# Performance work log

Hardware: AMD Instinct MI355X
Metric: run time of the kernel (lower is better)

## Reference

```python
import jax, jax.numpy as jnp
import numpy as np

EPS = 1e-5
QB = 128.0  # 2**(bit-1), bit=8

def _int8_wrap(q):
    # Emulate torch's .to(torch.int8) two's-complement wrap (e.g. 128 -> -128).
    return jnp.mod(q + 128.0, 256.0) - 128.0

def setup_inputs() -> dict:
    key = jax.random.key(0)
    k1, k2, k3 = jax.random.split(key, 3)
    x = jax.random.normal(k1, (4, 2048, 2048), dtype=jnp.float32)
    weights = jax.random.normal(k2, (8192, 2048), dtype=jnp.float32)
    bias = jax.random.normal(k3, (8192,), dtype=jnp.float32)
    return {"x": x, "weights": weights, "bias": bias}

def reference(x, weights, bias):
    in_features = x.shape[-1]
    out_features = weights.shape[0]
    # LayerNorm over last dim, no affine (F.layer_norm defaults, eps=1e-5)
    mu = jnp.mean(x, axis=-1, keepdims=True)
    var = jnp.mean(jnp.square(x - mu), axis=-1, keepdims=True)
    input_norm = (x - mu) * jax.lax.rsqrt(var + EPS)
    # absmax int8 activation quant (nl_next=False path)
    max_val = jnp.max(jnp.abs(input_norm))
    q = _int8_wrap(jnp.round(input_norm * (QB / max_val)))
    dequant = max_val / QB
    # weight sign-binarization around the mean
    weight_quant = jnp.sign(weights - jnp.mean(weights))
    # quantized matmul + dequant scales + bias
    out = jnp.einsum('bsd,od->bso', q, weight_quant)  # [B,S,out]
    beta = jnp.sum(jnp.abs(weights)) / (in_features * out_features)
    out = out * (dequant * beta) + bias
    return out
```

## Files before the change

kernel.cpp:

```cpp
#include <hip/hip_runtime.h>


using i32x4 = __attribute__((ext_vector_type(4))) int;

typedef const __attribute__((address_space(1))) void cg_void;
typedef __attribute__((address_space(3))) void lds_void;

#define K_DIM 2048
#define N_DIM 8192
#define M_DIM 8192
#define NELEM_W 16777216


__global__ __launch_bounds__(256) void pass1(const float* __restrict__ x,
                                             const float4* __restrict__ w4,
                                             float* __restrict__ mu_arr,
                                             float* __restrict__ rstd_arr,
                                             float* __restrict__ rowmax,
                                             double2* __restrict__ part) {
    __shared__ double sbd[8];
    __shared__ float sb1[4];
    __shared__ float sb2[8];
    const int bid = blockIdx.x, t = threadIdx.x;
    const int lane = t & 63, wv = t >> 6;
    if (bid < 1024) {
        double s = 0.0, a = 0.0;
        for (int i = bid * 256 + t; i < NELEM_W / 4; i += 1024 * 256) {
            float4 v = w4[i];
            s += (double)v.x + (double)v.y + (double)v.z + (double)v.w;
            a += fabs((double)v.x) + fabs((double)v.y) + fabs((double)v.z) + fabs((double)v.w);
        }
        for (int o = 32; o; o >>= 1) { s += __shfl_xor(s, o); a += __shfl_xor(a, o); }
        if (lane == 0) { sbd[wv] = s; sbd[4 + wv] = a; }
        __syncthreads();
        if (t == 0) {
            double2 r;
            r.x = sbd[0] + sbd[1] + sbd[2] + sbd[3];
            r.y = sbd[4] + sbd[5] + sbd[6] + sbd[7];
            part[bid] = r;
        }
    } else {
        const int row = bid - 1024;
        const float4* xr = (const float4*)x + (size_t)row * 512;
        float4 v0 = xr[t], v1 = xr[t + 256];
        float s = v0.x + v0.y + v0.z + v0.w + v1.x + v1.y + v1.z + v1.w;
        for (int o = 32; o; o >>= 1) s += __shfl_xor(s, o);
        if (lane == 0) sb1[wv] = s;
        __syncthreads();
        float mu = (sb1[0] + sb1[1] + sb1[2] + sb1[3]) * (1.0f / 2048.0f);
        float ssq = 0.f, md = 0.f, d;
        d = v0.x - mu; ssq += d * d; md = fmaxf(md, fabsf(d));
        d = v0.y - mu; ssq += d * d; md = fmaxf(md, fabsf(d));
        d = v0.z - mu; ssq += d * d; md = fmaxf(md, fabsf(d));
        d = v0.w - mu; ssq += d * d; md = fmaxf(md, fabsf(d));
        d = v1.x - mu; ssq += d * d; md = fmaxf(md, fabsf(d));
        d = v1.y - mu; ssq += d * d; md = fmaxf(md, fabsf(d));
        d = v1.z - mu; ssq += d * d; md = fmaxf(md, fabsf(d));
        d = v1.w - mu; ssq += d * d; md = fmaxf(md, fabsf(d));
        for (int o = 32; o; o >>= 1) {
            ssq += __shfl_xor(ssq, o);
            md = fmaxf(md, __shfl_xor(md, o));
        }
        if (lane == 0) { sb2[wv] = ssq; sb2[4 + wv] = md; }
        __syncthreads();
        if (t == 0) {
            float var = (sb2[0] + sb2[1] + sb2[2] + sb2[3]) * (1.0f / 2048.0f);
            float rstd = 1.0f / sqrtf(var + 1e-5f);
            mu_arr[row] = mu;
            rstd_arr[row] = rstd;
            rowmax[row] = fmaxf(fmaxf(sb2[4], sb2[5]), fmaxf(sb2[6], sb2[7])) * rstd;
        }
    }
}

__global__ __launch_bounds__(256) void wred2(const double2* __restrict__ part,
                                             const float* __restrict__ rowmax,
                                             unsigned* __restrict__ scal) {
    double s = 0.0, a = 0.0;
    float m = 0.f;
    const int t = threadIdx.x, lane = t & 63, wv = t >> 6;
    for (int i = t; i < 1024; i += 256) { double2 p = part[i]; s += p.x; a += p.y; }
    for (int i = t; i < 8192; i += 256) m = fmaxf(m, rowmax[i]);
    for (int o = 32; o; o >>= 1) {
        s += __shfl_xor(s, o); a += __shfl_xor(a, o);
        m = fmaxf(m, __shfl_xor(m, o));
    }
    __shared__ double sbd[8];
    __shared__ float sbm[4];
    if (lane == 0) { sbd[wv] = s; sbd[4 + wv] = a; sbm[wv] = m; }
    __syncthreads();
    if (t == 0) {
        double st = sbd[0] + sbd[1] + sbd[2] + sbd[3];
        double at = sbd[4] + sbd[5] + sbd[6] + sbd[7];
        ((float*)scal)[0] = fmaxf(fmaxf(sbm[0], sbm[1]), fmaxf(sbm[2], sbm[3]));
        ((float*)scal)[1] = (float)(st / (double)NELEM_W);
        ((float*)scal)[2] = (float)(at / (double)NELEM_W);
    }
}

__device__ __forceinline__ int sgn8(float d) { return (d > 0.f) ? 1 : ((d < 0.f) ? -1 : 0); }

__global__ __launch_bounds__(256) void pass2(const float* __restrict__ x,
                                             const float4* __restrict__ w4,
                                             const float* __restrict__ mu_arr,
                                             const float* __restrict__ rstd_arr,
                                             const unsigned* __restrict__ scal,
                                             signed char* __restrict__ q,
                                             int4* __restrict__ wq4) {
    const int bid = blockIdx.x, t = threadIdx.x;
    if (bid < 1024) {
        float wm = ((const float*)scal)[1];
        for (int i = bid * 256 + t; i < NELEM_W / 16; i += 1024 * 256) {
            int words[4];
            #pragma unroll
            for (int jj = 0; jj < 4; ++jj) {
                float4 v = w4[i * 4 + jj];
                int b0 = sgn8(v.x - wm) & 255, b1 = sgn8(v.y - wm) & 255;
                int b2 = sgn8(v.z - wm) & 255, b3 = sgn8(v.w - wm) & 255;
                words[jj] = b0 | (b1 << 8) | (b2 << 16) | (b3 << 24);
            }
            wq4[i] = make_int4(words[0], words[1], words[2], words[3]);
        }
    } else {
        const int row = bid - 1024;
        float mu = mu_arr[row], rstd = rstd_arr[row];
        float s = 128.0f / ((const float*)scal)[0];
        const float4* xr = (const float4*)x + (size_t)row * 512;
        float4 v0 = xr[2 * t], v1 = xr[2 * t + 1];
        float xs[8] = {v0.x, v0.y, v0.z, v0.w, v1.x, v1.y, v1.z, v1.w};
        int b[8];
        #pragma unroll
        for (int j = 0; j < 8; ++j) {
            float norm = (xs[j] - mu) * rstd;
            int qi = (int)rintf(norm * s);
            b[j] = qi & 255;
        }
        int w0 = b[0] | (b[1] << 8) | (b[2] << 16) | (b[3] << 24);
        int w1 = b[4] | (b[5] << 8) | (b[6] << 16) | (b[7] << 24);
        ((int2*)(q + (size_t)row * 2048))[t] = make_int2(w0, w1);
    }
}

#define LD16(p) (*(const i32x4*)(p))

#define STAGE(aoff, boff, sbase)                                                            \
    do {                                                                                    \
        _Pragma("unroll") for (int i_ = 0; i_ < 4; ++i_)                                    \
            __builtin_amdgcn_global_load_lds((cg_void*)(gA + (size_t)i_ * 131072 + (aoff)), \
                (lds_void*)(lds + (sbase) + i_ * 8192 + w * 1024), 16, 0, 0);               \
        _Pragma("unroll") for (int i_ = 0; i_ < 4; ++i_)                                    \
            __builtin_amdgcn_global_load_lds((cg_void*)(gB + (size_t)i_ * 131072 + (boff)), \
                (lds_void*)(lds + (sbase) + 32768 + i_ * 8192 + w * 1024), 16, 0, 0);       \
    } while (0)

#define MFC(MB, AF, BF)                                                                     \
    __builtin_amdgcn_s_setprio(1);                                                          \
    _Pragma("unroll") for (int mm = 0; mm < 4; ++mm)                                        \
        _Pragma("unroll") for (int nn = 0; nn < 4; ++nn)                                    \
            acc[(MB) + mm][nn] = __builtin_amdgcn_mfma_i32_16x16x64_i8(                     \
                AF[mm], BF[nn], acc[(MB) + mm][nn], 0, 0, 0);                               \
    __builtin_amdgcn_s_setprio(0);

__global__ __launch_bounds__(512, 2) void gemm_i8(const signed char* __restrict__ A,
                                                  const signed char* __restrict__ B,
                                                  const float* __restrict__ bias,
                                                  const unsigned* __restrict__ scal,
                                                  float* __restrict__ C) {
    __shared__ alignas(16) char lds[131072];
    const int t = threadIdx.x, w = t >> 6, lane = t & 63;

    const int wg = blockIdx.x;
    const int xcd = wg & 7, j = wg >> 3;
    const int bm = (xcd * 4 + (j >> 3)) * 256;
    const int col0 = (j & 7) * 4;

    const int wr = w >> 2, wc = w & 3;
    const int r16 = lane & 15, ko = lane >> 4;

    const int srow = w * 8 + (lane >> 3);
    const int scol = ((lane & 7) ^ (lane >> 3)) << 4;
    const signed char* gA = A + (size_t)(bm + srow) * K_DIM + scol;
    const signed char* gB = B + (size_t)(col0 * 256 + srow) * K_DIM + scol;

    const char* aBase = lds + (wr * 128 + r16) * 128;
    const char* bBase = lds + 32768 + (wc * 64 + r16) * 128;
    const int xr = (r16 & 7) << 4;
    const int sw0 = (ko * 16) ^ xr;
    const int sw1 = (64 + ko * 16) ^ xr;

    const float scale = (((const float*)scal)[0] * (1.0f / 128.0f)) * ((const float*)scal)[2];

    i32x4 acc[8][4] = {};
    i32x4 a0[4], a1[4], b0[4], b1[4];

    STAGE(0, 0, 0);

    #pragma unroll 2
    for (int gt = 0; gt < 64; ++gt) {
        const int c = (gt & 1) << 16;
        if (gt < 63) {
            const int nt = gt + 1;
            const int kt1 = nt & 15, rep1 = nt >> 4;
            const size_t aoff = (size_t)(kt1 * 128);
            const size_t boff = (size_t)rep1 * 524288 + (size_t)(kt1 * 128);
            STAGE(aoff, boff, (nt & 1) << 16);
            asm volatile("s_waitcnt vmcnt(8)" ::: "memory");
        } else {
            asm volatile("s_waitcnt vmcnt(0)" ::: "memory");
        }
        __builtin_amdgcn_s_barrier();

        #pragma unroll
        for (int m = 0; m < 4; ++m) a0[m] = LD16(aBase + c + m * 2048 + sw0);
        #pragma unroll
        for (int n = 0; n < 4; ++n) b0[n] = LD16(bBase + c + n * 2048 + sw0);
        #pragma unroll
        for (int m = 0; m < 4; ++m) a1[m] = LD16(aBase + c + (4 + m) * 2048 + sw0);
        MFC(0, a0, b0);
        #pragma unroll
        for (int m = 0; m < 4; ++m) a0[m] = LD16(aBase + c + m * 2048 + sw1);
        #pragma unroll
        for (int n = 0; n < 4; ++n) b1[n] = LD16(bBase + c + n * 2048 + sw1);
        MFC(4, a1, b0);
        #pragma unroll
        for (int m = 0; m < 4; ++m) a1[m] = LD16(aBase + c + (4 + m) * 2048 + sw1);
        MFC(0, a0, b1);
        MFC(4, a1, b1);
        __builtin_amdgcn_s_barrier();

        if ((gt & 15) == 15) {
            const int rep = gt >> 4;
            const int colbase = (col0 + rep) * 256 + wc * 64;
            float bi[4];
            #pragma unroll
            for (int n = 0; n < 4; ++n) bi[n] = bias[colbase + n * 16 + r16];
            #pragma unroll
            for (int m = 0; m < 8; ++m) {
                #pragma unroll
                for (int n = 0; n < 4; ++n) {
                    #pragma unroll
                    for (int r = 0; r < 4; ++r) {
                        int row = bm + wr * 128 + m * 16 + ko * 4 + r;
                        int col = colbase + n * 16 + r16;
                        C[(size_t)row * N_DIM + col] = (float)acc[m][n][r] * scale + bi[n];
                    }
                }
            }
            #pragma unroll
            for (int m = 0; m < 8; ++m)
                #pragma unroll
                for (int n = 0; n < 4; ++n) acc[m][n] = (i32x4){0, 0, 0, 0};
        }
    }
}

extern "C" void kernel_launch(void* const* d_in, const int* in_sizes, int n_in,
                              void* d_out, int out_size, void* d_ws, size_t ws_size,
                              hipStream_t stream) {
    const float* x = (const float*)d_in[0];
    const float* wts = (const float*)d_in[1];
    const float* bias = (const float*)d_in[2];
    float* out = (float*)d_out;

    char* ws = (char*)d_ws;
    unsigned* scal = (unsigned*)ws;
    double2* part = (double2*)(ws + 1024);
    float* mu = (float*)(ws + 32768);
    float* rstd = (float*)(ws + 65536);
    float* rowmax = (float*)(ws + 98304);
    signed char* q = (signed char*)(ws + 131072);
    signed char* wq = (signed char*)(ws + 131072 + 16777216);

    hipLaunchKernelGGL(pass1, dim3(9216), dim3(256), 0, stream,
                       x, (const float4*)wts, mu, rstd, rowmax, part);
    hipLaunchKernelGGL(wred2, dim3(1), dim3(256), 0, stream, part, rowmax, scal);
    hipLaunchKernelGGL(pass2, dim3(9216), dim3(256), 0, stream,
                       x, (const float4*)wts, mu, rstd, scal, q, (int4*)wq);
    hipLaunchKernelGGL(gemm_i8, dim3(256), dim3(512), 0, stream,
                       q, wq, bias, scal, out);
}
```

Measured before the change: 253.4 us.

## Switch int8 GEMM to 32x32x32 MFMA with barrier-separated K phases

Replaces the 16x16x64 int8 MFMA tiling with 32x32x32 int8 MFMAs accumulating into 16-wide vectors. The per-wave tile stays 128x64 but uses fewer, larger instructions and fewer fragment loads. Each 128-wide K slice is split into four phases, each with an LDS fragment load, a full lgkmcnt wait and a workgroup barrier. The larger MFMA is meant to raise throughput per LDS byte, but the extra barriers and waits limit overlap of LDS reads with math. The epilogue row and column mapping is rewritten for the 32x32 output layout.

```diff
diff --git a/kernel.cpp b/kernel.cpp
--- a/kernel.cpp
+++ b/kernel.cpp
@@ -2,6 +2,7 @@
 
 
 using i32x4 = __attribute__((ext_vector_type(4))) int;
+using i32x16 = __attribute__((ext_vector_type(16))) int;
 
 typedef const __attribute__((address_space(1))) void cg_void;
 typedef __attribute__((address_space(3))) void lds_void;
@@ -153,13 +154,22 @@
                 (lds_void*)(lds + (sbase) + 32768 + i_ * 8192 + w * 1024), 16, 0, 0);       \
     } while (0)
 
-#define MFC(MB, AF, BF)                                                                     \
-    __builtin_amdgcn_s_setprio(1);                                                          \
-    _Pragma("unroll") for (int mm = 0; mm < 4; ++mm)                                        \
-        _Pragma("unroll") for (int nn = 0; nn < 4; ++nn)                                    \
-            acc[(MB) + mm][nn] = __builtin_amdgcn_mfma_i32_16x16x64_i8(                     \
-                AF[mm], BF[nn], acc[(MB) + mm][nn], 0, 0, 0);                               \
-    __builtin_amdgcn_s_setprio(0);
+#define PHASE32(KOFF, LEAD_BAR)                                                             \
+    do {                                                                                    \
+        _Pragma("unroll") for (int mb = 0; mb < 4; ++mb)                                    \
+            af[mb] = LD16(aB + mb * 4096 + (KOFF));                                         \
+        _Pragma("unroll") for (int nb = 0; nb < 2; ++nb)                                    \
+            bf[nb] = LD16(bB + nb * 4096 + (KOFF));                                         \
+        if (LEAD_BAR) __builtin_amdgcn_s_barrier();                                         \
+        asm volatile("s_waitcnt lgkmcnt(0)" ::: "memory");                                  \
+        __builtin_amdgcn_s_setprio(1);                                                      \
+        _Pragma("unroll") for (int mb = 0; mb < 4; ++mb)                                    \
+            _Pragma("unroll") for (int nb = 0; nb < 2; ++nb)                                 \
+                acc[mb][nb] = __builtin_amdgcn_mfma_i32_32x32x32_i8(                        \
+                    af[mb], bf[nb], acc[mb][nb], 0, 0, 0);                                  \
+        __builtin_amdgcn_s_setprio(0);                                                      \
+        __builtin_amdgcn_s_barrier();                                                       \
+    } while (0)
 
 __global__ __launch_bounds__(512, 2) void gemm_i8(const signed char* __restrict__ A,
                                                   const signed char* __restrict__ B,
@@ -175,23 +185,25 @@
     const int col0 = (j & 7) * 4;
 
     const int wr = w >> 2, wc = w & 3;
-    const int r16 = lane & 15, ko = lane >> 4;
+    const int r32 = lane & 31, hi = lane >> 5;
 
     const int srow = w * 8 + (lane >> 3);
     const int scol = ((lane & 7) ^ (lane >> 3)) << 4;
     const signed char* gA = A + (size_t)(bm + srow) * K_DIM + scol;
     const signed char* gB = B + (size_t)(col0 * 256 + srow) * K_DIM + scol;
 
-    const char* aBase = lds + (wr * 128 + r16) * 128;
-    const char* bBase = lds + 32768 + (wc * 64 + r16) * 128;
-    const int xr = (r16 & 7) << 4;
-    const int sw0 = (ko * 16) ^ xr;
-    const int sw1 = (64 + ko * 16) ^ xr;
+    const char* aBase = lds + (wr * 128 + r32) * 128;
+    const char* bBase = lds + 32768 + (wc * 64 + r32) * 128;
+    const int xr32 = (r32 & 7) << 4;
+    const int kf0 = (0 * 32 + hi * 16) ^ xr32;
+    const int kf1 = (1 * 32 + hi * 16) ^ xr32;
+    const int kf2 = (2 * 32 + hi * 16) ^ xr32;
+    const int kf3 = (3 * 32 + hi * 16) ^ xr32;
 
     const float scale = (((const float*)scal)[0] * (1.0f / 128.0f)) * ((const float*)scal)[2];
 
-    i32x4 acc[8][4] = {};
-    i32x4 a0[4], a1[4], b0[4], b1[4];
+    i32x16 acc[4][2] = {};
+    i32x4 af[4], bf[2];
 
     STAGE(0, 0, 0);
 
@@ -210,46 +222,35 @@
         }
         __builtin_amdgcn_s_barrier();
 
-        #pragma unroll
-        for (int m = 0; m < 4; ++m) a0[m] = LD16(aBase + c + m * 2048 + sw0);
-        #pragma unroll
-        for (int n = 0; n < 4; ++n) b0[n] = LD16(bBase + c + n * 2048 + sw0);
-        #pragma unroll
-        for (int m = 0; m < 4; ++m) a1[m] = LD16(aBase + c + (4 + m) * 2048 + sw0);
-        MFC(0, a0, b0);
-        #pragma unroll
-        for (int m = 0; m < 4; ++m) a0[m] = LD16(aBase + c + m * 2048 + sw1);
-        #pragma unroll
-        for (int n = 0; n < 4; ++n) b1[n] = LD16(bBase + c + n * 2048 + sw1);
-        MFC(4, a1, b0);
-        #pragma unroll
-        for (int m = 0; m < 4; ++m) a1[m] = LD16(aBase + c + (4 + m) * 2048 + sw1);
-        MFC(0, a0, b1);
-        MFC(4, a1, b1);
-        __builtin_amdgcn_s_barrier();
+        const char* aB = aBase + c;
+        const char* bB = bBase + c;
+        PHASE32(kf0, 0);
+        PHASE32(kf1, 1);
+        PHASE32(kf2, 1);
+        PHASE32(kf3, 1);
 
         if ((gt & 15) == 15) {
             const int rep = gt >> 4;
             const int colbase = (col0 + rep) * 256 + wc * 64;
-            float bi[4];
-            #pragma unroll
-            for (int n = 0; n < 4; ++n) bi[n] = bias[colbase + n * 16 + r16];
-            #pragma unroll
-            for (int m = 0; m < 8; ++m) {
+            float bi[2];
+            #pragma unroll
+            for (int nb = 0; nb < 2; ++nb) bi[nb] = bias[colbase + nb * 32 + r32];
+            #pragma unroll
+            for (int mb = 0; mb < 4; ++mb) {
                 #pragma unroll
-                for (int n = 0; n < 4; ++n) {
+                for (int nb = 0; nb < 2; ++nb) {
                     #pragma unroll
-                    for (int r = 0; r < 4; ++r) {
-                        int row = bm + wr * 128 + m * 16 + ko * 4 + r;
-                        int col = colbase + n * 16 + r16;
-                        C[(size_t)row * N_DIM + col] = (float)acc[m][n][r] * scale + bi[n];
+                    for (int r = 0; r < 16; ++r) {
+                        int row = bm + wr * 128 + mb * 32 + (r & 3) + 8 * (r >> 2) + 4 * hi;
+                        int col = colbase + nb * 32 + r32;
+                        C[(size_t)row * N_DIM + col] = (float)acc[mb][nb][r] * scale + bi[nb];
                     }
                 }
             }
             #pragma unroll
-            for (int m = 0; m < 8; ++m)
+            for (int mb = 0; mb < 4; ++mb)
                 #pragma unroll
-                for (int n = 0; n < 4; ++n) acc[m][n] = (i32x4){0, 0, 0, 0};
+                for (int nb = 0; nb < 2; ++nb) acc[mb][nb] = (i32x16){};
         }
     }
 }
```

After: 255.6 us. No clear change (+0.9%).

## Retile int8 GEMM to 256x128 blocks with 32x32x32 MFMA and higher occupancy

Applied to the files above, without the earlier changes.

Replaces the persistent 256x1024 block tiling (256 blocks looping over four 256-column sweeps, 128 KB LDS) with 2048 smaller blocks of 256x128 output and a K-step of 64, using 48 KB LDS and launch bounds allowing four blocks per CU. The inner product switches from 16x16x64 to 32x32x32 int8 MFMA with a new swizzle and 64-byte LDS rows, and the epilogue runs once after the K loop. The aim is more resident waves to hide memory latency and simpler scheduling. In exchange, operand reuse per LDS byte drops and the B matrix is reloaded by many more blocks, raising global and L2 traffic.

```diff
diff --git a/kernel.cpp b/kernel.cpp
--- a/kernel.cpp
+++ b/kernel.cpp
@@ -2,6 +2,7 @@
 
 
 using i32x4 = __attribute__((ext_vector_type(4))) int;
+using i32x16 = __attribute__((ext_vector_type(16))) int;
 
 typedef const __attribute__((address_space(1))) void cg_void;
 typedef __attribute__((address_space(3))) void lds_void;
@@ -142,114 +143,102 @@
 }
 
 #define LD16(p) (*(const i32x4*)(p))
-
-#define STAGE(aoff, boff, sbase)                                                            \
+#define TILE_BYTES 24576
+
+#define STAGE(koff, sbase)                                                                  \
     do {                                                                                    \
-        _Pragma("unroll") for (int i_ = 0; i_ < 4; ++i_)                                    \
-            __builtin_amdgcn_global_load_lds((cg_void*)(gA + (size_t)i_ * 131072 + (aoff)), \
-                (lds_void*)(lds + (sbase) + i_ * 8192 + w * 1024), 16, 0, 0);               \
-        _Pragma("unroll") for (int i_ = 0; i_ < 4; ++i_)                                    \
-            __builtin_amdgcn_global_load_lds((cg_void*)(gB + (size_t)i_ * 131072 + (boff)), \
-                (lds_void*)(lds + (sbase) + 32768 + i_ * 8192 + w * 1024), 16, 0, 0);       \
+        __builtin_amdgcn_global_load_lds((cg_void*)(gA + (koff)),                           \
+            (lds_void*)(lds + (sbase) + w * 2048), 16, 0, 0);                               \
+        __builtin_amdgcn_global_load_lds((cg_void*)(gA + 16 * K_DIM + (koff)),              \
+            (lds_void*)(lds + (sbase) + w * 2048 + 1024), 16, 0, 0);                        \
+        __builtin_amdgcn_global_load_lds((cg_void*)(gB + (koff)),                           \
+            (lds_void*)(lds + (sbase) + 16384 + w * 1024), 16, 0, 0);                       \
     } while (0)
 
-#define MFC(MB, AF, BF)                                                                     \
-    __builtin_amdgcn_s_setprio(1);                                                          \
-    _Pragma("unroll") for (int mm = 0; mm < 4; ++mm)                                        \
-        _Pragma("unroll") for (int nn = 0; nn < 4; ++nn)                                    \
-            acc[(MB) + mm][nn] = __builtin_amdgcn_mfma_i32_16x16x64_i8(                     \
-                AF[mm], BF[nn], acc[(MB) + mm][nn], 0, 0, 0);                               \
-    __builtin_amdgcn_s_setprio(0);
-
-__global__ __launch_bounds__(512, 2) void gemm_i8(const signed char* __restrict__ A,
+__global__ __launch_bounds__(512, 4) void gemm_i8(const signed char* __restrict__ A,
                                                   const signed char* __restrict__ B,
                                                   const float* __restrict__ bias,
                                                   const unsigned* __restrict__ scal,
                                                   float* __restrict__ C) {
-    __shared__ alignas(16) char lds[131072];
+    __shared__ alignas(16) char lds[49152];
     const int t = threadIdx.x, w = t >> 6, lane = t & 63;
 
     const int wg = blockIdx.x;
-    const int xcd = wg & 7, j = wg >> 3;
-    const int bm = (xcd * 4 + (j >> 3)) * 256;
-    const int col0 = (j & 7) * 4;
-
-    const int wr = w >> 2, wc = w & 3;
-    const int r16 = lane & 15, ko = lane >> 4;
-
-    const int srow = w * 8 + (lane >> 3);
-    const int scol = ((lane & 7) ^ (lane >> 3)) << 4;
-    const signed char* gA = A + (size_t)(bm + srow) * K_DIM + scol;
-    const signed char* gB = B + (size_t)(col0 * 256 + srow) * K_DIM + scol;
-
-    const char* aBase = lds + (wr * 128 + r16) * 128;
-    const char* bBase = lds + 32768 + (wc * 64 + r16) * 128;
-    const int xr = (r16 & 7) << 4;
-    const int sw0 = (ko * 16) ^ xr;
-    const int sw1 = (64 + ko * 16) ^ xr;
+    const int xcd = wg & 7, idx = wg >> 3;
+    const int bm = (xcd * 4 + (idx >> 6)) * 256;
+    const int bn = (idx & 63) * 128;
+
+    const int wr = w >> 1, wc = w & 1;
+    const int r32 = lane & 31, hi = lane >> 5;
+
+    const int srow = lane >> 2;
+    const int scol = ((lane & 3) ^ ((lane >> 3) & 3)) << 4;
+    const signed char* gA = A + (size_t)(bm + w * 32 + srow) * K_DIM + scol;
+    const signed char* gB = B + (size_t)(bn + w * 16 + srow) * K_DIM + scol;
+
+    const char* aBase = lds + (wr * 64 + r32) * 64;
+    const char* bBase = lds + 16384 + (wc * 64 + r32) * 64;
+    const int swz = ((r32 >> 1) & 3) << 4;
+    const int sw0 = (hi * 16) ^ swz;
+    const int sw1 = (32 + hi * 16) ^ swz;
 
     const float scale = (((const float*)scal)[0] * (1.0f / 128.0f)) * ((const float*)scal)[2];
 
-    i32x4 acc[8][4] = {};
-    i32x4 a0[4], a1[4], b0[4], b1[4];
-
-    STAGE(0, 0, 0);
+    i32x16 acc[2][2] = {};
+    i32x4 a0[2], a1[2], b0[2], b1[2];
+
+    STAGE(0, 0);
 
     #pragma unroll 2
-    for (int gt = 0; gt < 64; ++gt) {
-        const int c = (gt & 1) << 16;
-        if (gt < 63) {
-            const int nt = gt + 1;
-            const int kt1 = nt & 15, rep1 = nt >> 4;
-            const size_t aoff = (size_t)(kt1 * 128);
-            const size_t boff = (size_t)rep1 * 524288 + (size_t)(kt1 * 128);
-            STAGE(aoff, boff, (nt & 1) << 16);
-            asm volatile("s_waitcnt vmcnt(8)" ::: "memory");
+    for (int kt = 0; kt < 32; ++kt) {
+        const int c = (kt & 1) * TILE_BYTES;
+        if (kt < 31) {
+            STAGE((kt + 1) * 64, ((kt + 1) & 1) * TILE_BYTES);
+            asm volatile("s_waitcnt vmcnt(3)" ::: "memory");
         } else {
             asm volatile("s_waitcnt vmcnt(0)" ::: "memory");
         }
         __builtin_amdgcn_s_barrier();
 
         #pragma unroll
-        for (int m = 0; m < 4; ++m) a0[m] = LD16(aBase + c + m * 2048 + sw0);
-        #pragma unroll
-        for (int n = 0; n < 4; ++n) b0[n] = LD16(bBase + c + n * 2048 + sw0);
-        #pragma unroll
-        for (int m = 0; m < 4; ++m) a1[m] = LD16(aBase + c + (4 + m) * 2048 + sw0);
-        MFC(0, a0, b0);
-        #pragma unroll
-        for (int m = 0; m < 4; ++m) a0[m] = LD16(aBase + c + m * 2048 + sw1);
-        #pragma unroll
-        for (int n = 0; n < 4; ++n) b1[n] = LD16(bBase + c + n * 2048 + sw1);
-        MFC(4, a1, b0);
-        #pragma unroll
-        for (int m = 0; m < 4; ++m) a1[m] = LD16(aBase + c + (4 + m) * 2048 + sw1);
-        MFC(0, a0, b1);
-        MFC(4, a1, b1);
+        for (int mb = 0; mb < 2; ++mb) a0[mb] = LD16(aBase + c + mb * 2048 + sw0);
+        #pragma unroll
+        for (int nb = 0; nb < 2; ++nb) b0[nb] = LD16(bBase + c + nb * 2048 + sw0);
+        #pragma unroll
+        for (int mb = 0; mb < 2; ++mb) a1[mb] = LD16(aBase + c + mb * 2048 + sw1);
+        #pragma unroll
+        for (int nb = 0; nb < 2; ++nb) b1[nb] = LD16(bBase + c + nb * 2048 + sw1);
+        __builtin_amdgcn_s_setprio(1);
+        #pragma unroll
+        for (int mb = 0; mb < 2; ++mb)
+            #pragma unroll
+            for (int nb = 0; nb < 2; ++nb)
+                acc[mb][nb] = __builtin_amdgcn_mfma_i32_32x32x32_i8(a0[mb], b0[nb],
+                                                                    acc[mb][nb], 0, 0, 0);
+        #pragma unroll
+        for (int mb = 0; mb < 2; ++mb)
+            #pragma unroll
+            for (int nb = 0; nb < 2; ++nb)
+                acc[mb][nb] = __builtin_amdgcn_mfma_i32_32x32x32_i8(a1[mb], b1[nb],
+                                                                    acc[mb][nb], 0, 0, 0);
+        __builtin_amdgcn_s_setprio(0);
         __builtin_amdgcn_s_barrier();
-
-        if ((gt & 15) == 15) {
-            const int rep = gt >> 4;
-            const int colbase = (col0 + rep) * 256 + wc * 64;
-            float bi[4];
-            #pragma unroll
-            for (int n = 0; n < 4; ++n) bi[n] = bias[colbase + n * 16 + r16];
-            #pragma unroll
-            for (int m = 0; m < 8; ++m) {
-                #pragma unroll
-                for (int n = 0; n < 4; ++n) {
-                    #pragma unroll
-                    for (int r = 0; r < 4; ++r) {
-                        int row = bm + wr * 128 + m * 16 + ko * 4 + r;
-                        int col = colbase + n * 16 + r16;
-                        C[(size_t)row * N_DIM + col] = (float)acc[m][n][r] * scale + bi[n];
-                    }
-                }
+    }
+
+    const int colbase = bn + wc * 64;
+    float bi[2];
+    #pragma unroll
+    for (int nb = 0; nb < 2; ++nb) bi[nb] = bias[colbase + nb * 32 + r32];
+    #pragma unroll
+    for (int mb = 0; mb < 2; ++mb) {
+        #pragma unroll
+        for (int nb = 0; nb < 2; ++nb) {
+            #pragma unroll
+            for (int r = 0; r < 16; ++r) {
+                int row = bm + wr * 64 + mb * 32 + (r & 3) + 8 * (r >> 2) + 4 * hi;
+                int col = colbase + nb * 32 + r32;
+                C[(size_t)row * N_DIM + col] = (float)acc[mb][nb][r] * scale + bi[nb];
             }
-            #pragma unroll
-            for (int m = 0; m < 8; ++m)
-                #pragma unroll
-                for (int n = 0; n < 4; ++n) acc[m][n] = (i32x4){0, 0, 0, 0};
         }
     }
 }
@@ -276,6 +265,6 @@
     hipLaunchKernelGGL(wred2, dim3(1), dim3(256), 0, stream, part, rowmax, scal);
     hipLaunchKernelGGL(pass2, dim3(9216), dim3(256), 0, stream,
                        x, (const float4*)wts, mu, rstd, scal, q, (int4*)wq);
-    hipLaunchKernelGGL(gemm_i8, dim3(256), dim3(512), 0, stream,
+    hipLaunchKernelGGL(gemm_i8, dim3(2048), dim3(512), 0, stream,
                        q, wq, bias, scal, out);
 }
```

After: 227.7 us, median of 2. -10.1%, faster.
